# Performance work log

Measured on AMD Instinct MI355X. Metric: run time of the kernel, lower is better.

The kernel has to match this reference:

```python
import jax, jax.numpy as jnp
import numpy as np

B, N, DIM, DFF, CLS = 8, 1024, 768, 3072, 1

def setup_inputs() -> dict:
    key = jax.random.key(0)
    ks = jax.random.split(key, 12)
    x = jax.random.normal(ks[0], (B, N + CLS, DIM), dtype=jnp.float32)
    y = jax.random.normal(ks[1], (B, N + CLS, DIM), dtype=jnp.float32)
    coords = jax.random.uniform(ks[2], (N, N, 6), dtype=jnp.float32)
    U = jax.random.normal(ks[3], (DIM, DIM), dtype=jnp.float32) * (DIM ** -0.5)  # xavier-ish
    S1 = jax.random.uniform(ks[4], (DIM,), dtype=jnp.float32)
    S2 = jax.random.uniform(ks[5], (DIM,), dtype=jnp.float32)
    gating = jnp.asarray(1.0, dtype=jnp.float32)
    h_temp = jnp.asarray(0.1, dtype=jnp.float32)
    p_temp = jnp.asarray(1.0, dtype=jnp.float32)
    pos_emb = jax.random.uniform(ks[6], (N, 6, 1), dtype=jnp.float32)  # trunc_normal in [0,1]
    W1 = jax.random.normal(ks[7], (2 * DIM, DFF), dtype=jnp.float32) * 0.02
    b1 = jnp.zeros((DFF,), dtype=jnp.float32)
    W2 = jax.random.normal(ks[8], (DFF, DIM), dtype=jnp.float32) * 0.02
    b2 = jnp.zeros((DIM,), dtype=jnp.float32)
    return {"x": x, "y": y, "coords": coords, "U": U, "S1": S1, "S2": S2,
            "gating": gating, "h_temp": h_temp, "p_temp": p_temp, "pos_emb": pos_emb,
            "W1": W1, "b1": b1, "W2": W2, "b2": b2}

def reference(x, y, coords, U, S1, S2, gating, h_temp, p_temp, pos_emb, W1, b1, W2, b2):
    scale = DIM ** -0.5  # a_temp=False -> python float constant
    xb = x[:, CLS:, :]          # [B,N,D] (layer_norm=False -> Identity)
    yb = y[:, CLS:, :]
    y_cls = y[:, :CLS, :]
    # SpectralDecomp: x @ U.T @ diag(|S|) @ U, two spectra stacked -> [B,2,N,D]
    t = xb @ U.T
    xs = jnp.stack([(t * jnp.abs(S1)) @ U, (t * jnp.abs(S2)) @ U], axis=1)
    patch = jax.nn.softmax(jnp.einsum('bknd,bmd->bknm', xs, yb) * scale, axis=-1)  # [B,2,N,N]
    pos_logits = -jnp.abs(p_temp) * jnp.einsum('ijc,ic->ij', coords, pos_emb[..., 0])  # [N,N]
    pos = jax.nn.softmax(pos_logits, axis=-1)[None, None]  # broadcast to [B,2,N,N]
    g = jax.nn.sigmoid(gating)
    attn = (1.0 - g) * patch + g * pos  # [B,2,N,N]
    # entropy heat-map + hard routing
    entropy = jnp.sum(-attn * jnp.log(attn + 1e-8), axis=-1).transpose(0, 2, 1)  # [B,N,2]
    hmap = 2.0 - 2.0 * jax.nn.sigmoid(h_temp * entropy)
    fgbg = hmap[..., 0] >= hmap[..., 1]
    route = jnp.stack([fgbg, ~fgbg], axis=-1).astype(hmap.dtype)  # [B,N,2] one-hot
    heat_map = jnp.sum(hmap * route, axis=-1, keepdims=True)  # [B,N,1]
    attn_c = jnp.einsum('bkij,bik->bij', attn, route)  # route-weighted combine -> [B,N,N]
    y_out = attn_c @ yb  # [B,N,D]
    y_full = jnp.concatenate([y_cls, y_out], axis=1)  # [B,N+1,D]
    # proj MLP on concat(x, y)
    h = jnp.concatenate([x, y_full], axis=-1) @ W1 + b1
    xp = jax.nn.gelu(h, approximate=False) @ W2 + b2
    xp = jnp.concatenate([xp[:, :CLS], heat_map * xp[:, CLS:]], axis=1)
    return x + xp
```

## Files before the change

### kernel.cpp

```cpp
#include <hip/hip_runtime.h>
#include <hip/hip_bf16.h>
#include <math.h>

#define BB   8
#define NTOK 1024
#define DIM  768
#define DFF  3072
#define NP1  1025

typedef __bf16 bf16x8 __attribute__((ext_vector_type(8)));
typedef float  f32x4  __attribute__((ext_vector_type(4)));
typedef float  f32x16 __attribute__((ext_vector_type(16)));

__device__ __forceinline__ float waveMax(float v){
  #pragma unroll
  for (int o = 32; o > 0; o >>= 1) v = fmaxf(v, __shfl_down(v, o, 64));
  return v;
}
__device__ __forceinline__ float waveSum(float v){
  #pragma unroll
  for (int o = 32; o > 0; o >>= 1) v += __shfl_down(v, o, 64);
  return v;
}
__device__ __forceinline__ float blockMax(float v, float* red){
  int lane = threadIdx.x & 63, w = threadIdx.x >> 6;
  v = waveMax(v);
  if (lane == 0) red[w] = v;
  __syncthreads();
  float r = fmaxf(fmaxf(red[0], red[1]), fmaxf(red[2], red[3]));
  __syncthreads();
  return r;
}
__device__ __forceinline__ float blockSum(float v, float* red){
  int lane = threadIdx.x & 63, w = threadIdx.x >> 6;
  v = waveSum(v);
  if (lane == 0) red[w] = v;
  __syncthreads();
  float r = red[0] + red[1] + red[2] + red[3];
  __syncthreads();
  return r;
}

__global__ __launch_bounds__(256) void pos_kernel(
    const float* __restrict__ coords, const float* __restrict__ pos_emb,
    const float* __restrict__ p_temp, float* __restrict__ pos)
{
  int i = blockIdx.x;
  int tid = threadIdx.x;
  __shared__ float red[4];
  __shared__ float pe[6];
  if (tid < 6) pe[tid] = pos_emb[i*6 + tid];
  __syncthreads();
  float pt = fabsf(p_temp[0]);
  float v[4]; float mx = -INFINITY;
  #pragma unroll
  for (int j = 0; j < 4; j++){
    int jj = tid + j*256;
    const float* c = coords + ((long long)i*NTOK + jj)*6;
    float d = c[0]*pe[0] + c[1]*pe[1] + c[2]*pe[2] + c[3]*pe[3] + c[4]*pe[4] + c[5]*pe[5];
    v[j] = -pt * d;
    mx = fmaxf(mx, v[j]);
  }
  mx = blockMax(mx, red);
  float s = 0.f;
  #pragma unroll
  for (int j = 0; j < 4; j++){ v[j] = __expf(v[j] - mx); s += v[j]; }
  s = blockSum(s, red);
  float inv = 1.f / s;
  #pragma unroll
  for (int j = 0; j < 4; j++) pos[(long long)i*NTOK + tid + j*256] = v[j] * inv;
}

__global__ __launch_bounds__(256) void rowproc_kernel(
    const __hip_bfloat16* __restrict__ S,
    const float* __restrict__ pos,
    __hip_bfloat16* __restrict__ attnc,
    float* __restrict__ heat,
    const float* __restrict__ gating, const float* __restrict__ h_temp)
{
  int row = blockIdx.x;
  int b = row >> 10, i = row & 1023;
  int tid = threadIdx.x;
  __shared__ __align__(16) float a0[NTOK];
  __shared__ __align__(16) float a1[NTOK];
  __shared__ float red[4];
  float g = 1.f / (1.f + __expf(-gating[0]));
  float ht = h_temp[0];
  float ent[2];
  const int c0 = tid * 4;
  f32x4 pv = *(const f32x4*)&pos[(long long)i*NTOK + c0];
  #pragma unroll
  for (int k = 0; k < 2; k++){
    const __hip_bfloat16* Sr = S + ((long long)((k*8 + b)*NTOK) + i) * NTOK;
    union { uint2 u; __hip_bfloat16 h[4]; } ld;
    ld.u = *(const uint2*)&Sr[c0];
    f32x4 v;
    #pragma unroll
    for (int j = 0; j < 4; j++) v[j] = __bfloat162float(ld.h[j]);
    float mx = fmaxf(fmaxf(v[0], v[1]), fmaxf(v[2], v[3]));
    mx = blockMax(mx, red);
    float s = 0.f;
    #pragma unroll
    for (int j = 0; j < 4; j++){ v[j] = __expf(v[j] - mx); s += v[j]; }
    s = blockSum(s, red);
    float inv = 1.f / s;
    float e = 0.f;
    float* arow = k ? a1 : a0;
    f32x4 at;
    #pragma unroll
    for (int j = 0; j < 4; j++){
      at[j] = (1.f - g) * (v[j] * inv) + g * pv[j];
      e += -at[j] * __logf(at[j] + 1e-8f);
    }
    *(f32x4*)&arow[c0] = at;
    ent[k] = blockSum(e, red);
  }
  float h0 = 2.f - 2.f / (1.f + __expf(-ht * ent[0]));
  float h1 = 2.f - 2.f / (1.f + __expf(-ht * ent[1]));
  bool fg = (h0 >= h1);
  if (tid == 0) heat[row] = fg ? h0 : h1;
  const float* sel = fg ? a0 : a1;
  f32x4 sv = *(const f32x4*)&sel[c0];
  union { __hip_bfloat16 h[4]; uint2 u; } pk;
  #pragma unroll
  for (int j = 0; j < 4; j++) pk.h[j] = __float2bfloat16(sv[j]);
  *(uint2*)(attnc + ((long long)b*NTOK + i)*NTOK + c0) = pk.u;
}

__global__ __launch_bounds__(256) void conv_xy_kernel(
    const float* __restrict__ x, const float* __restrict__ y, __hip_bfloat16* __restrict__ xy)
{
  long long idx = (long long)blockIdx.x*256 + threadIdx.x;
  int d = (int)(idx % DIM);
  long long br = idx / DIM;
  int r = (int)(br % NP1);
  xy[br*1536 + d] = __float2bfloat16(x[idx]);
  if (r == 0) xy[br*1536 + DIM + d] = __float2bfloat16(y[idx]);
}

__global__ __launch_bounds__(256) void transpose_conv_kernel(
    const float* __restrict__ in, long long sIn, int ldin,
    __hip_bfloat16* __restrict__ outT, long long sT,
    __hip_bfloat16* __restrict__ outS, long long sS,
    int R, int C,
    const float* __restrict__ sc1, const float* __restrict__ sc2,
    __hip_bfloat16* __restrict__ outT1, __hip_bfloat16* __restrict__ outT2)
{
  __shared__ float tile[32][33];
  int bx = blockIdx.x, by = blockIdx.y, z = blockIdx.z;
  const float* inb = in + (long long)z*sIn;
  int tx = threadIdx.x & 31, ty = threadIdx.x >> 5;
  #pragma unroll
  for (int p = 0; p < 4; p++){
    int r = by*32 + p*8 + ty;
    int c = bx*32 + tx;
    float v = inb[(long long)r*ldin + c];
    tile[p*8 + ty][tx] = v;
    if (outS) outS[(long long)z*sS + (long long)r*C + c] = __float2bfloat16(v);
  }
  __syncthreads();
  #pragma unroll
  for (int p = 0; p < 4; p++){
    int c = bx*32 + p*8 + ty;
    int r = by*32 + tx;
    float v = tile[tx][p*8 + ty];
    long long oidx = (long long)z*sT + (long long)c*R + r;
    outT[oidx] = __float2bfloat16(v);
    if (outT1) outT1[(long long)c*R + r] = __float2bfloat16(v * fabsf(sc1[r]));
    if (outT2) outT2[(long long)c*R + r] = __float2bfloat16(v * fabsf(sc2[r]));
  }
}

__device__ __forceinline__ void async16(const __bf16* gp, __bf16* lp){
  __builtin_amdgcn_global_load_lds(
      (const __attribute__((address_space(1))) void*)gp,
      (__attribute__((address_space(3))) void*)lp, 16, 0, 0);
}

template<int EPI>
__global__ __launch_bounds__(256) void mfma_gemm(
    const __bf16* __restrict__ A, const __bf16* __restrict__ Bm, void* __restrict__ Cv,
    int M, int N, int K, int lda, int ldb, int ldc,
    long long sAz, long long sBz, long long sCz,
    int maskA, int shiftB, int maskB, float alpha,
    const float* __restrict__ bias,
    const float* __restrict__ xres,
    const float* __restrict__ heat)
{
  __shared__ __align__(16) __bf16 Atile[128*64];
  __shared__ __align__(16) __bf16 Btile[128*64];

  const int tid  = threadIdx.x;
  const int lane = tid & 63;
  const int wv   = tid >> 6;
  const int wr   = wv >> 1, wc = wv & 1;
  const int n0 = blockIdx.x * 128, m0 = blockIdx.y * 128;
  const int z  = blockIdx.z;

  const __bf16* Ab = A  + (long long)(z & maskA) * sAz;
  const __bf16* Bb = Bm + (long long)((z >> shiftB) & maskB) * sBz;

  const __bf16* gA[4]; const __bf16* gB[4];
  __bf16 *lA[4], *lB[4];
  #pragma unroll
  for (int i = 0; i < 4; i++){
    int s0  = (i*4 + wv) * 64;
    int s   = s0 + lane;
    int row = s >> 3;
    int kc  = (s & 7) ^ (row & 7);
    int gm = m0 + row; if (gm > M-1) gm = M-1;
    int gn = n0 + row; if (gn > N-1) gn = N-1;
    gA[i] = Ab + (long long)gm * lda + kc * 8;
    gB[i] = Bb + (long long)gn * ldb + kc * 8;
    lA[i] = &Atile[s0 * 8];
    lB[i] = &Btile[s0 * 8];
  }

  const int fm = lane & 31;
  const int kq = lane >> 5;
  const __bf16* pA[2][4]; const __bf16* pB[2][4];
  #pragma unroll
  for (int rr = 0; rr < 2; rr++){
    int rowA = wr*64 + rr*32 + fm;
    int rowB = wc*64 + rr*32 + fm;
    #pragma unroll
    for (int st = 0; st < 4; st++){
      pA[rr][st] = &Atile[rowA*64 + ((st*2 + kq) ^ (rowA & 7)) * 8];
      pB[rr][st] = &Btile[rowB*64 + ((st*2 + kq) ^ (rowB & 7)) * 8];
    }
  }

  f32x16 acc[2][2] = {};

  for (int k0 = 0; k0 < K; k0 += 64){
    __syncthreads();
    #pragma unroll
    for (int i = 0; i < 4; i++){ async16(gA[i], lA[i]); async16(gB[i], lB[i]); }
    #pragma unroll
    for (int i = 0; i < 4; i++){ gA[i] += 64; gB[i] += 64; }
    __syncthreads();
    #pragma unroll
    for (int st = 0; st < 4; st++){
      bf16x8 a0 = *(const bf16x8*)pA[0][st];
      bf16x8 a1 = *(const bf16x8*)pA[1][st];
      bf16x8 b0 = *(const bf16x8*)pB[0][st];
      bf16x8 b1 = *(const bf16x8*)pB[1][st];
      acc[0][0] = __builtin_amdgcn_mfma_f32_32x32x16_bf16(a0, b0, acc[0][0], 0, 0, 0);
      acc[0][1] = __builtin_amdgcn_mfma_f32_32x32x16_bf16(a0, b1, acc[0][1], 0, 0, 0);
      acc[1][0] = __builtin_amdgcn_mfma_f32_32x32x16_bf16(a1, b0, acc[1][0], 0, 0, 0);
      acc[1][1] = __builtin_amdgcn_mfma_f32_32x32x16_bf16(a1, b1, acc[1][1], 0, 0, 0);
    }
  }

  const int col_l = lane & 31;
  const int row_q = (lane >> 5) * 4;
  #pragma unroll
  for (int r = 0; r < 2; r++){
    #pragma unroll
    for (int c = 0; c < 2; c++){
      int gn  = n0 + wc*64 + c*32 + col_l;
      if (gn >= N) continue;
      int gmb = m0 + wr*64 + r*32 + row_q;
      f32x16 v = acc[r][c];
      #pragma unroll
      for (int g = 0; g < 4; g++){
        #pragma unroll
        for (int q = 0; q < 4; q++){
          int gm = gmb + g*8 + q;
          if (gm >= M) continue;
          float cval = alpha * v[g*4 + q];
          long long cidx = (long long)z*sCz + (long long)gm*ldc + gn;
          if (EPI == 1){
            ((__hip_bfloat16*)Cv)[cidx] = __float2bfloat16(cval);
          } else if (EPI == 2){
            float h = cval + bias[gn];
            float ge = 0.5f * h * (1.f + erff(h * 0.70710678118654752f));
            ((__hip_bfloat16*)Cv)[cidx] = __float2bfloat16(ge);
          } else {
            float h = cval + bias[gn];
            int bq = gm / NP1;
            int rr2 = gm - bq * NP1;
            float f = (rr2 == 0) ? 1.f : heat[bq*NTOK + (rr2 - 1)];
            ((float*)Cv)[cidx] = xres[cidx] + f * h;
          }
        }
      }
    }
  }
}

extern "C" void kernel_launch(void* const* d_in, const int* in_sizes, int n_in,
                              void* d_out, int out_size, void* d_ws, size_t ws_size,
                              hipStream_t stream)
{
  const float* x       = (const float*)d_in[0];
  const float* y       = (const float*)d_in[1];
  const float* coords  = (const float*)d_in[2];
  const float* U       = (const float*)d_in[3];
  const float* S1      = (const float*)d_in[4];
  const float* S2      = (const float*)d_in[5];
  const float* gating  = (const float*)d_in[6];
  const float* h_temp  = (const float*)d_in[7];
  const float* p_temp  = (const float*)d_in[8];
  const float* pos_emb = (const float*)d_in[9];
  const float* W1      = (const float*)d_in[10];
  const float* b1      = (const float*)d_in[11];
  const float* W2      = (const float*)d_in[12];
  const float* b2      = (const float*)d_in[13];
  float* out = (float*)d_out;
  char* ws = (char*)d_ws;

  size_t off = 0;
  auto alloc = [&](size_t bytes){ size_t r = off; off = (off + bytes + 255) & ~(size_t)255; return r; };
  const long long NN  = (long long)NTOK * NTOK;
  const long long DD  = (long long)DIM * DIM;
  const size_t o_pos  = alloc(NN * 4);
  const size_t o_S    = alloc((size_t)BB*NP1*DFF * 2);
  const size_t o_xy   = alloc((size_t)BB*NP1*1536 * 2);
  const size_t o_yb   = alloc((size_t)BB*NTOK*DIM * 2);
  const size_t o_ybT  = alloc((size_t)BB*DIM*NTOK * 2);
  const size_t o_xs   = alloc((size_t)2*BB*NTOK*DIM * 2);
  const size_t o_attn = alloc((size_t)BB*NN * 2);
  const size_t o_UT   = alloc((size_t)DD * 2);
  const size_t o_UTs  = alloc((size_t)2*DD * 2);
  const size_t o_Mk   = alloc((size_t)2*DD * 2);
  const size_t o_W1T  = alloc((size_t)DFF*2*DIM * 2);
  const size_t o_W2T  = alloc((size_t)DIM*DFF * 2);
  const size_t o_heat = alloc((size_t)BB*NTOK * 4);

  __hip_bfloat16* S_bf = (__hip_bfloat16*)(ws + o_S);
  __hip_bfloat16* hg   = (__hip_bfloat16*)(ws + o_S);
  __hip_bfloat16* xy   = (__hip_bfloat16*)(ws + o_xy);
  __hip_bfloat16* yb   = (__hip_bfloat16*)(ws + o_yb);
  __hip_bfloat16* ybT  = (__hip_bfloat16*)(ws + o_ybT);
  __hip_bfloat16* xs   = (__hip_bfloat16*)(ws + o_xs);
  __hip_bfloat16* attnc= (__hip_bfloat16*)(ws + o_attn);
  __hip_bfloat16* UT   = (__hip_bfloat16*)(ws + o_UT);
  __hip_bfloat16* UTs  = (__hip_bfloat16*)(ws + o_UTs);
  __hip_bfloat16* Mk   = (__hip_bfloat16*)(ws + o_Mk);
  __hip_bfloat16* W1T  = (__hip_bfloat16*)(ws + o_W1T);
  __hip_bfloat16* W2T  = (__hip_bfloat16*)(ws + o_W2T);
  float* pos  = (float*)(ws + o_pos);
  float* heat = (float*)(ws + o_heat);

  const float scale = 0.03608439182435161f;
  dim3 blk(256);

  pos_kernel<<<dim3(NTOK), blk, 0, stream>>>(coords, pos_emb, p_temp, pos);
  conv_xy_kernel<<<dim3((BB*NP1*DIM)/256), blk, 0, stream>>>(x, y, xy);
  transpose_conv_kernel<<<dim3(DIM/32, DIM/32, 1), blk, 0, stream>>>(
      U, 0LL, DIM, UT, 0LL, nullptr, 0LL, DIM, DIM, S1, S2, UTs, UTs + DD);
  transpose_conv_kernel<<<dim3(DFF/32, (2*DIM)/32, 1), blk, 0, stream>>>(
      W1, 0LL, DFF, W1T, 0LL, nullptr, 0LL, 2*DIM, DFF, nullptr, nullptr, nullptr, nullptr);
  transpose_conv_kernel<<<dim3(DIM/32, DFF/32, 1), blk, 0, stream>>>(
      W2, 0LL, DIM, W2T, 0LL, nullptr, 0LL, DFF, DIM, nullptr, nullptr, nullptr, nullptr);
  transpose_conv_kernel<<<dim3(DIM/32, NTOK/32, BB), blk, 0, stream>>>(
      y + DIM, (long long)NP1*DIM, DIM, ybT, (long long)DIM*NTOK, yb, (long long)NTOK*DIM,
      NTOK, DIM, nullptr, nullptr, nullptr, nullptr);

  mfma_gemm<1><<<dim3(DIM/128, DIM/128, 2), blk, 0, stream>>>(
      (const __bf16*)UT, (const __bf16*)UTs, Mk,
      DIM, DIM, DIM, DIM, DIM, DIM,
      0LL, DD, DD, 0, 0, 1, 1.f, nullptr, nullptr, nullptr);

  mfma_gemm<1><<<dim3(DIM/128, NTOK/128, 16), blk, 0, stream>>>(
      (const __bf16*)(xy + 1536), (const __bf16*)Mk, xs,
      NTOK, DIM, DIM, 1536, DIM, DIM,
      (long long)NP1*1536, DD, (long long)NTOK*DIM,
      7, 3, 1, 1.f, nullptr, nullptr, nullptr);

  mfma_gemm<1><<<dim3(NTOK/128, NTOK/128, 16), blk, 0, stream>>>(
      (const __bf16*)xs, (const __bf16*)yb, S_bf,
      NTOK, NTOK, DIM, DIM, DIM, NTOK,
      (long long)NTOK*DIM, (long long)NTOK*DIM, NN,
      15, 0, 7, scale, nullptr, nullptr, nullptr);

  rowproc_kernel<<<dim3(BB*NTOK), blk, 0, stream>>>(S_bf, pos, attnc, heat, gating, h_temp);

  mfma_gemm<1><<<dim3(DIM/128, NTOK/128, BB), blk, 0, stream>>>(
      (const __bf16*)attnc, (const __bf16*)ybT, xy + 1536 + DIM,
      NTOK, DIM, NTOK, NTOK, NTOK, 1536,
      NN, (long long)DIM*NTOK, (long long)NP1*1536,
      7, 0, 7, 1.f, nullptr, nullptr, nullptr);

  mfma_gemm<2><<<dim3(DFF/128, (BB*NP1 + 127)/128, 1), blk, 0, stream>>>(
      (const __bf16*)xy, (const __bf16*)W1T, hg,
      BB*NP1, DFF, 2*DIM, 1536, 1536, DFF,
      0LL, 0LL, 0LL, 0, 0, 0, 1.f, b1, nullptr, nullptr);

  mfma_gemm<3><<<dim3(DIM/128, (BB*NP1 + 127)/128, 1), blk, 0, stream>>>(
      (const __bf16*)hg, (const __bf16*)W2T, out,
      BB*NP1, DIM, DFF, DFF, DFF, DIM,
      0LL, 0LL, 0LL, 0, 0, 0, 1.f, b2, x, heat);
}
```

Baseline: 540.2 us.

## Double-buffer GEMM LDS tiles with async prefetch and use tanh GELU

Splits the GEMM shared-memory tiles into two K=32 stages and prefetches the next stage with async global-to-LDS loads while MFMAs consume the current one, aiming to hide global load latency behind compute. Also replaces the exact erf GELU in the first MLP epilogue with the tanh approximation using a fast exp, reducing epilogue math cost. The approximation deviates slightly from the reference's exact GELU, and the pipelined loop assumes an even number of K stages.

```diff
diff --git a/kernel.cpp b/kernel.cpp
--- a/kernel.cpp
+++ b/kernel.cpp
@@ -187,8 +187,8 @@
     const float* __restrict__ xres,
     const float* __restrict__ heat)
 {
-  __shared__ __align__(16) __bf16 Atile[128*64];
-  __shared__ __align__(16) __bf16 Btile[128*64];
+  __shared__ __align__(16) __bf16 Atile[2][128*32];
+  __shared__ __align__(16) __bf16 Btile[2][128*32];
 
   const int tid  = threadIdx.x;
   const int lane = tid & 63;
@@ -200,68 +200,86 @@
   const __bf16* Ab = A  + (long long)(z & maskA) * sAz;
   const __bf16* Bb = Bm + (long long)((z >> shiftB) & maskB) * sBz;
 
-  const __bf16* gA[4]; const __bf16* gB[4];
-  __bf16 *lA[4], *lB[4];
-  #pragma unroll
-  for (int i = 0; i < 4; i++){
-    int s0  = (i*4 + wv) * 64;
+  const __bf16* gA[2]; const __bf16* gB[2];
+  __bf16 *lA0[2], *lA1[2], *lB0[2], *lB1[2];
+  #pragma unroll
+  for (int i = 0; i < 2; i++){
+    int s0  = i*256 + wv*64;
     int s   = s0 + lane;
-    int row = s >> 3;
-    int kc  = (s & 7) ^ (row & 7);
+    int row = s >> 2;
+    int kc  = (s & 3) ^ (row & 3);
     int gm = m0 + row; if (gm > M-1) gm = M-1;
     int gn = n0 + row; if (gn > N-1) gn = N-1;
     gA[i] = Ab + (long long)gm * lda + kc * 8;
     gB[i] = Bb + (long long)gn * ldb + kc * 8;
-    lA[i] = &Atile[s0 * 8];
-    lB[i] = &Btile[s0 * 8];
+    lA0[i] = &Atile[0][s0 * 8];  lA1[i] = &Atile[1][s0 * 8];
+    lB0[i] = &Btile[0][s0 * 8];  lB1[i] = &Btile[1][s0 * 8];
   }
 
   const int fm = lane & 31;
   const int kq = lane >> 5;
-  const __bf16* pA[2][4]; const __bf16* pB[2][4];
+  const __bf16* pA[2][2]; const __bf16* pB[2][2];
   #pragma unroll
   for (int rr = 0; rr < 2; rr++){
     int rowA = wr*64 + rr*32 + fm;
     int rowB = wc*64 + rr*32 + fm;
     #pragma unroll
-    for (int st = 0; st < 4; st++){
-      pA[rr][st] = &Atile[rowA*64 + ((st*2 + kq) ^ (rowA & 7)) * 8];
-      pB[rr][st] = &Btile[rowB*64 + ((st*2 + kq) ^ (rowB & 7)) * 8];
+    for (int st = 0; st < 2; st++){
+      pA[rr][st] = &Atile[0][rowA*32 + ((st*2 + kq) ^ (rowA & 3)) * 8];
+      pB[rr][st] = &Btile[0][rowB*32 + ((st*2 + kq) ^ (rowB & 3)) * 8];
     }
   }
 
   f32x16 acc[2][2] = {};
 
-  for (int k0 = 0; k0 < K; k0 += 64){
+  const int nIter = K >> 5;
+
+  #pragma unroll
+  for (int i = 0; i < 2; i++){ async16(gA[i], lA0[i]); async16(gB[i], lB0[i]); gA[i] += 32; gB[i] += 32; }
+
+  for (int t = 0; t < nIter; t += 2){
     __syncthreads();
     #pragma unroll
-    for (int i = 0; i < 4; i++){ async16(gA[i], lA[i]); async16(gB[i], lB[i]); }
-    #pragma unroll
-    for (int i = 0; i < 4; i++){ gA[i] += 64; gB[i] += 64; }
-    __syncthreads();
-    #pragma unroll
-    for (int st = 0; st < 4; st++){
-      bf16x8 a0 = *(const bf16x8*)pA[0][st];
-      bf16x8 a1 = *(const bf16x8*)pA[1][st];
-      bf16x8 b0 = *(const bf16x8*)pB[0][st];
-      bf16x8 b1 = *(const bf16x8*)pB[1][st];
+    for (int i = 0; i < 2; i++){ async16(gA[i], lA1[i]); async16(gB[i], lB1[i]); gA[i] += 32; gB[i] += 32; }
+    #pragma unroll
+    for (int st = 0; st < 2; st++){
+      bf16x8 b0 = *(const bf16x8*)(pB[0][st]);
+      bf16x8 b1 = *(const bf16x8*)(pB[1][st]);
+      bf16x8 a0 = *(const bf16x8*)(pA[0][st]);
+      bf16x8 a1 = *(const bf16x8*)(pA[1][st]);
       acc[0][0] = __builtin_amdgcn_mfma_f32_32x32x16_bf16(a0, b0, acc[0][0], 0, 0, 0);
       acc[0][1] = __builtin_amdgcn_mfma_f32_32x32x16_bf16(a0, b1, acc[0][1], 0, 0, 0);
       acc[1][0] = __builtin_amdgcn_mfma_f32_32x32x16_bf16(a1, b0, acc[1][0], 0, 0, 0);
       acc[1][1] = __builtin_amdgcn_mfma_f32_32x32x16_bf16(a1, b1, acc[1][1], 0, 0, 0);
     }
+    __syncthreads();
+    if (t + 2 < nIter){
+      #pragma unroll
+      for (int i = 0; i < 2; i++){ async16(gA[i], lA0[i]); async16(gB[i], lB0[i]); gA[i] += 32; gB[i] += 32; }
+    }
+    #pragma unroll
+    for (int st = 0; st < 2; st++){
+      bf16x8 b0 = *(const bf16x8*)(pB[0][st] + 4096);
+      bf16x8 b1 = *(const bf16x8*)(pB[1][st] + 4096);
+      bf16x8 a0 = *(const bf16x8*)(pA[0][st] + 4096);
+      bf16x8 a1 = *(const bf16x8*)(pA[1][st] + 4096);
+      acc[0][0] = __builtin_amdgcn_mfma_f32_32x32x16_bf16(a0, b0, acc[0][0], 0, 0, 0);
+      acc[0][1] = __builtin_amdgcn_mfma_f32_32x32x16_bf16(a0, b1, acc[0][1], 0, 0, 0);
+      acc[1][0] = __builtin_amdgcn_mfma_f32_32x32x16_bf16(a1, b0, acc[1][0], 0, 0, 0);
+      acc[1][1] = __builtin_amdgcn_mfma_f32_32x32x16_bf16(a1, b1, acc[1][1], 0, 0, 0);
+    }
   }
 
   const int col_l = lane & 31;
   const int row_q = (lane >> 5) * 4;
   #pragma unroll
-  for (int r = 0; r < 2; r++){
-    #pragma unroll
-    for (int c = 0; c < 2; c++){
-      int gn  = n0 + wc*64 + c*32 + col_l;
+  for (int rr = 0; rr < 2; rr++){
+    #pragma unroll
+    for (int cc = 0; cc < 2; cc++){
+      int gn  = n0 + wc*64 + cc*32 + col_l;
       if (gn >= N) continue;
-      int gmb = m0 + wr*64 + r*32 + row_q;
-      f32x16 v = acc[r][c];
+      int gmb = m0 + wr*64 + rr*32 + row_q;
+      f32x16 v = acc[rr][cc];
       #pragma unroll
       for (int g = 0; g < 4; g++){
         #pragma unroll
@@ -274,7 +292,9 @@
             ((__hip_bfloat16*)Cv)[cidx] = __float2bfloat16(cval);
           } else if (EPI == 2){
             float h = cval + bias[gn];
-            float ge = 0.5f * h * (1.f + erff(h * 0.70710678118654752f));
+            float u = 0.7978845608f * (h + 0.044715f * h * h * h);
+            float tt = 1.f - 2.f / (__expf(2.f * u) + 1.f);
+            float ge = 0.5f * h * (1.f + tt);
             ((__hip_bfloat16*)Cv)[cidx] = __float2bfloat16(ge);
           } else {
             float h = cval + bias[gn];
```

After: 625.0 us. 1.16x slower.
